# Performance work log

Hardware: AMD Instinct MI355X
Metric: run time of the kernel (lower is better)

The kernel has to match this reference:

```python
import jax, jax.numpy as jnp
import numpy as np

N, E, D, G = 50000, 600000, 128, 64
EPS = 1e-5


def prelu(x, a):
    return jnp.where(x >= 0, x, a * x)


def degree_norms(edge_src, edge_dst):
    ones = jnp.ones((E,), jnp.float32)
    deg_out = jax.ops.segment_sum(ones, edge_src, num_segments=N)
    deg_in = jax.ops.segment_sum(ones, edge_dst, num_segments=N)
    norm_src = jnp.where(deg_out > 0, jax.lax.rsqrt(jnp.maximum(deg_out, 1.0)), 0.0)
    norm_dst = jnp.where(deg_in > 0, jax.lax.rsqrt(jnp.maximum(deg_in, 1.0)), 0.0)
    return norm_src, norm_dst


def graph_conv(x, W, b, alpha, edge_src, edge_dst, norm_src, norm_dst):
    # DGL GraphConv norm='both': D_out^{-1/2} on src, aggregate, D_in^{-1/2} on dst, then linear
    xs = x * norm_src[:, None]
    agg = jax.ops.segment_sum(xs[edge_src], edge_dst, num_segments=N)
    agg = agg * norm_dst[:, None]
    h = agg @ W + b
    return prelu(h, alpha)


def batch_norm(h, gamma, beta):
    mean = jnp.mean(h, axis=0)
    var = jnp.mean(jnp.square(h - mean), axis=0)
    return (h - mean) * jax.lax.rsqrt(var + EPS) * gamma + beta


def setup_inputs() -> dict:
    key = jax.random.key(0)
    ks = jax.random.split(key, 8)
    inp = {
        "heat": jax.random.normal(ks[0], (N, D), jnp.float32),
        "edge_src": jax.random.randint(ks[1], (E,), 0, N, jnp.int32),
        "edge_dst": jax.random.randint(ks[2], (E,), 0, N, jnp.int32),
        "graph_ids": jnp.sort(jax.random.randint(ks[3], (N,), 0, G, jnp.int32)),
    }
    for i in range(2):
        kw = jax.random.fold_in(ks[4], i)
        inp[f"W{i}"] = jax.random.normal(kw, (D, D), jnp.float32) * (1.0 / np.sqrt(D))
        inp[f"b{i}"] = jnp.zeros((D,), jnp.float32)
        inp[f"ac{i}"] = jnp.float32(0.25)  # conv PReLU alpha
        inp[f"g{i}"] = jnp.ones((D,), jnp.float32)
        inp[f"be{i}"] = jnp.zeros((D,), jnp.float32)
        inp[f"aa{i}"] = jnp.float32(0.25)  # outer PReLU alpha
    return inp


def reference(heat, edge_src, edge_dst, graph_ids,
              W0, b0, ac0, g0, be0, aa0,
              W1, b1, ac1, g1, be1, aa1):
    norm_src, norm_dst = degree_norms(edge_src, edge_dst)
    x = heat  # dropout in eval mode -> identity
    h = graph_conv(x, W0, b0, ac0, edge_src, edge_dst, norm_src, norm_dst)
    h = prelu(batch_norm(h, g0, be0), aa0)
    gh = jax.ops.segment_sum(h, graph_ids, num_segments=G)
    h = graph_conv(h, W1, b1, ac1, edge_src, edge_dst, norm_src, norm_dst)
    h = prelu(batch_norm(h, g1, be1), aa1)
    gh = gh + jax.ops.segment_sum(h, graph_ids, num_segments=G)
    return h, gh
```

## Files before the change

### kernel.cpp

```cpp
#include <hip/hip_runtime.h>
#include <hip/hip_fp8.h>

#define NN 50000
#define NE 600000
#define DD 128
#define GG 64
#define EPS 1e-5f
#define CAP 64
#define HB 60
#define ECHUNK 10000
#define NPARTS 8
#define HALFP 6250
#define HWORDSP 3125
#define ZROW 50000
#define NBUILD ((NE + 255) / 256)
#define HB0 NBUILD
#define WB0 (NBUILD + NPARTS * HB)
#define NWTB 128
#define NPB (NN * 16 / 256)

typedef unsigned short u16;
typedef unsigned int u32;
typedef unsigned char u8;
typedef u16 u16x8 __attribute__((ext_vector_type(8)));
typedef u8 u8x16 __attribute__((ext_vector_type(16)));
typedef u8 u8x8 __attribute__((ext_vector_type(8)));
typedef short bf16x8 __attribute__((ext_vector_type(8)));
typedef float f32x4 __attribute__((ext_vector_type(4)));

__device__ __forceinline__ float bf2f(u16 v) {
    return __uint_as_float(((u32)v) << 16);
}
__device__ __forceinline__ u16 f2bf(float f) {
    u32 u = __float_as_uint(f);
    u += 0x7fff + ((u >> 16) & 1);
    return (u16)(u >> 16);
}
__device__ __forceinline__ float f8tof(u8 b) {
    __hip_fp8_e4m3 v;
    v.__x = b;
    return (float)v;
}
__device__ __forceinline__ u8 ftof8(float f) {
    return __hip_fp8_e4m3(f).__x;
}

__global__ __launch_bounds__(256) void k_prep(
        const int* __restrict__ src, const int* __restrict__ dst,
        u32* __restrict__ partials, int* __restrict__ cnt_in, u16* __restrict__ csr,
        const float* __restrict__ W0, const float* __restrict__ W1,
        u16* __restrict__ wtb, u8* __restrict__ xsb) {
    __shared__ u32 hc[HWORDSP];
    int blk = blockIdx.x;
    int t = threadIdx.x;
    if (blk < NBUILD) {
        int e = blk * 256 + t;
        if (e < NE) {
            int d = dst[e];
            int pos = atomicAdd(&cnt_in[d], 1);
            if (pos < CAP) csr[(size_t)d * CAP + pos] = (u16)src[e];
        }
        return;
    }
    if (blk >= WB0) {
        int gt = (blk - WB0) * 256 + t;
        int lay = gt >> 14;
        int rem = gt & 16383;
        int c = rem >> 7, k = rem & 127;
        const float* W = lay ? W1 : W0;
        wtb[lay * DD * DD + c * DD + k] = f2bf(W[k * DD + c]);
        if (gt < 16) {
            u8x8 z = {0, 0, 0, 0, 0, 0, 0, 0};
            *(u8x8*)(xsb + (size_t)ZROW * DD + gt * 8) = z;
        }
        return;
    }
    int hb = blk - HB0;
    int b = hb % HB, p = hb / HB;
    for (int i = t; i < HWORDSP; i += 256) hc[i] = 0;
    __syncthreads();
    int lo = p * HALFP;
    int e0 = b * ECHUNK;
    for (int e = e0 + t; e < e0 + ECHUNK; e += 256) {
        int s = src[e] - lo;
        if ((u32)s < (u32)HALFP) atomicAdd(&hc[s >> 1], 1u << ((s & 1) << 4));
    }
    __syncthreads();
    u32* outp = partials + (size_t)(p * HB + b) * HWORDSP;
    for (int i = t; i < HWORDSP; i += 256) outp[i] = hc[i];
}

__global__ __launch_bounds__(256) void k_scale_rows(
        const u32* __restrict__ partials, const float* __restrict__ x,
        float* __restrict__ norm_src, u8* __restrict__ xsb,
        float* __restrict__ gh, float* __restrict__ stats) {
    __shared__ float snorm[16];
    int blk = blockIdx.x;
    int t = threadIdx.x;
    if (blk < 32) {
        gh[blk * 256 + t] = 0.f;
    } else if (blk == 32) {
        stats[t] = 0.f;
        stats[256 + t] = 0.f;
    }
    int rb = blk * 16;
    int s = t >> 5, c = t & 31;
    int rA = rb + 2 * s;
    int p = rA / HALFP;
    int j = (rA - p * HALFP) >> 1;
    u32 sum = 0;
    for (int b = c; b < HB; b += 32)
        sum += partials[(size_t)(p * HB + b) * HWORDSP + j];
    sum += __shfl_xor((int)sum, 1);
    sum += __shfl_xor((int)sum, 2);
    sum += __shfl_xor((int)sum, 4);
    sum += __shfl_xor((int)sum, 8);
    sum += __shfl_xor((int)sum, 16);
    if (c == 0) {
        u32 c0 = sum & 0xffffu, c1 = sum >> 16;
        float n0 = c0 ? rsqrtf((float)c0) : 0.f;
        float n1 = c1 ? rsqrtf((float)c1) : 0.f;
        snorm[2 * s] = n0;
        snorm[2 * s + 1] = n1;
        norm_src[rA] = n0;
        norm_src[rA + 1] = n1;
    }
    __syncthreads();
    int idx = blk * 256 + t;
    int row = idx >> 4;
    int c8 = (idx & 15) << 3;
    float ns = snorm[t >> 4];
    const float4* xp = (const float4*)(x + (size_t)row * DD + c8);
    float4 a = xp[0], b2 = xp[1];
    u8x8 o;
    o[0] = ftof8(a.x * ns); o[1] = ftof8(a.y * ns); o[2] = ftof8(a.z * ns); o[3] = ftof8(a.w * ns);
    o[4] = ftof8(b2.x * ns); o[5] = ftof8(b2.y * ns); o[6] = ftof8(b2.z * ns); o[7] = ftof8(b2.w * ns);
    *(u8x8*)(xsb + (size_t)row * DD + c8) = o;
}

#define LOADF8(v, ii)                                                    \
    u8x16 v##0 = *(const u8x16*)(xcol + (size_t)(ii)[0] * DD);           \
    u8x16 v##1 = *(const u8x16*)(xcol + (size_t)(ii)[1] * DD);           \
    u8x16 v##2 = *(const u8x16*)(xcol + (size_t)(ii)[2] * DD);           \
    u8x16 v##3 = *(const u8x16*)(xcol + (size_t)(ii)[3] * DD);           \
    u8x16 v##4 = *(const u8x16*)(xcol + (size_t)(ii)[4] * DD);           \
    u8x16 v##5 = *(const u8x16*)(xcol + (size_t)(ii)[5] * DD);           \
    u8x16 v##6 = *(const u8x16*)(xcol + (size_t)(ii)[6] * DD);           \
    u8x16 v##7 = *(const u8x16*)(xcol + (size_t)(ii)[7] * DD);

#define ACCF8(acc, v)                                                    \
    _Pragma("unroll")                                                    \
    for (int j = 0; j < 16; ++j) {                                       \
        float a01 = f8tof(v##0[j]) + f8tof(v##1[j]);                     \
        float a23 = f8tof(v##2[j]) + f8tof(v##3[j]);                     \
        float a45 = f8tof(v##4[j]) + f8tof(v##5[j]);                     \
        float a67 = f8tof(v##6[j]) + f8tof(v##7[j]);                     \
        acc[j] += (a01 + a23) + (a45 + a67);                             \
    }

__global__ __launch_bounds__(256) void k_gg(
        const u8* __restrict__ xsb, const int* __restrict__ cnt_in,
        const u16* __restrict__ csr,
        const u16* __restrict__ wtb, const float* __restrict__ bias,
        const float* __restrict__ ac, u16* __restrict__ hpreb,
        float* __restrict__ sums, float* __restrict__ sumsq) {
    __shared__ u16 sAg[4][16][DD + 8];
    __shared__ float sStat[2][4][DD];
    int t = threadIdx.x;
    int w = t >> 6;
    int l = t & 63;
    int rb = blockIdx.x * 64 + w * 16;
    bool wvalid = (rb < NN);
    int cl8 = l & 7;
    int rw = l >> 3;
    const u8* xcol = xsb + cl8 * 16;

    if (wvalid) {
#pragma unroll
        for (int gp = 0; gp < 2; ++gp) {
            int r = rb + gp * 8 + rw;
            int craw = cnt_in[r];
            int cnt = min(craw, CAP);
            const u16* ce = csr + (size_t)r * CAP;
            float acc[16];
#pragma unroll
            for (int j = 0; j < 16; ++j) acc[j] = 0.f;
            int e = 0;
            for (; e + 8 <= cnt; e += 8) {
                u16x8 ii = *(const u16x8*)(ce + e);
                LOADF8(va, ii)
                ACCF8(acc, va)
            }
            if (e < cnt) {
                u16x8 ii = *(const u16x8*)(ce + e);
                int jj[8];
#pragma unroll
                for (int j = 0; j < 8; ++j) jj[j] = (e + j < cnt) ? (int)ii[j] : ZROW;
                LOADF8(vm, jj)
                ACCF8(acc, vm)
            }
            float nd = craw > 0 ? rsqrtf((float)craw) : 0.f;
            u16x8 o0, o1;
#pragma unroll
            for (int j = 0; j < 8; ++j) {
                o0[j] = f2bf(acc[j] * nd);
                o1[j] = f2bf(acc[8 + j] * nd);
            }
            *(u16x8*)&sAg[w][gp * 8 + rw][cl8 * 16] = o0;
            *(u16x8*)&sAg[w][gp * 8 + rw][cl8 * 16 + 8] = o1;
        }
    }
    __syncthreads();

    int lr = l & 15;
    int kg = l >> 4;
    float alpha = ac[0];

    bf16x8 afrag[4];
    if (wvalid) {
        const u16* abase = &sAg[w][lr][kg * 8];
        afrag[0] = *(const bf16x8*)(abase);
        afrag[1] = *(const bf16x8*)(abase + 32);
        afrag[2] = *(const bf16x8*)(abase + 64);
        afrag[3] = *(const bf16x8*)(abase + 96);
    }

#pragma unroll
    for (int ct = 0; ct < 8; ++ct) {
        int c = ct * 16;
        float sS = 0.f, sQ = 0.f;
        if (wvalid) {
            const u16* bbase = wtb + (size_t)(c + lr) * DD + kg * 8;
            bf16x8 b0 = *(const bf16x8*)(bbase);
            bf16x8 b1 = *(const bf16x8*)(bbase + 32);
            bf16x8 b2 = *(const bf16x8*)(bbase + 64);
            bf16x8 b3 = *(const bf16x8*)(bbase + 96);
            float bv = bias[c + lr];
            f32x4 acc = {bv, bv, bv, bv};
            acc = __builtin_amdgcn_mfma_f32_16x16x32_bf16(afrag[0], b0, acc, 0, 0, 0);
            acc = __builtin_amdgcn_mfma_f32_16x16x32_bf16(afrag[1], b1, acc, 0, 0, 0);
            acc = __builtin_amdgcn_mfma_f32_16x16x32_bf16(afrag[2], b2, acc, 0, 0, 0);
            acc = __builtin_amdgcn_mfma_f32_16x16x32_bf16(afrag[3], b3, acc, 0, 0, 0);
#pragma unroll
            for (int j = 0; j < 4; ++j) {
                float h = acc[j];
                h = h >= 0.f ? h : alpha * h;
                u16 hb = f2bf(h);
                float hq = bf2f(hb);
                int grow = rb + kg * 4 + j;
                hpreb[(size_t)grow * DD + c + lr] = hb;
                sS += hq;
                sQ += hq * hq;
            }
        }
        sS += __shfl_xor(sS, 16); sS += __shfl_xor(sS, 32);
        sQ += __shfl_xor(sQ, 16); sQ += __shfl_xor(sQ, 32);
        if (kg == 0) {
            sStat[0][w][c + lr] = sS;
            sStat[1][w][c + lr] = sQ;
        }
    }
    __syncthreads();
    if (t < DD) {
        float s = sStat[0][0][t] + sStat[0][1][t] + sStat[0][2][t] + sStat[0][3][t];
        atomicAdd(&sums[t], s);
    } else if (t < 2 * DD) {
        int c = t - DD;
        float q = sStat[1][0][c] + sStat[1][1][c] + sStat[1][2][c] + sStat[1][3][c];
        atomicAdd(&sumsq[c], q);
    }
}

__global__ __launch_bounds__(256) void k_post(
        const u16* __restrict__ hpreb,
        const float* __restrict__ sums, const float* __restrict__ sumsq,
        const float* __restrict__ gamma, const float* __restrict__ beta,
        const float* __restrict__ aa, const float* __restrict__ nsrc,
        float* __restrict__ h_out, u8* __restrict__ xs_next, int lastLayer,
        const int* __restrict__ gids, float* __restrict__ gh) {
    __shared__ float sc[DD], sh[DD];
    __shared__ float red[2][DD];
    int t = threadIdx.x;
    if (t < DD) {
        float mean = sums[t] * (1.0f / NN);
        float var = sumsq[t] * (1.0f / NN) - mean * mean;
        float inv = rsqrtf(var + EPS);
        float s = inv * gamma[t];
        sc[t] = s;
        sh[t] = beta[t] - mean * s;
    }
    __syncthreads();
    float a = aa[0];
    int blk = blockIdx.x;

    if (blk < NPB) {
        int idx = blk * 256 + t;
        int row = idx >> 4;
        int c8 = (idx & 15) << 3;
        u16x8 hv = *(const u16x8*)(hpreb + (size_t)idx * 8);
        float v[8];
#pragma unroll
        for (int j = 0; j < 8; ++j) v[j] = bf2f(hv[j]) * sc[c8 + j] + sh[c8 + j];
#pragma unroll
        for (int j = 0; j < 8; ++j) v[j] = v[j] >= 0.f ? v[j] : a * v[j];
        if (lastLayer) {
            float4* op = (float4*)(h_out + (size_t)idx * 8);
            op[0] = make_float4(v[0], v[1], v[2], v[3]);
            op[1] = make_float4(v[4], v[5], v[6], v[7]);
        } else {
            float ns = nsrc[row];
            u8x8 o;
#pragma unroll
            for (int j = 0; j < 8; ++j) o[j] = ftof8(v[j] * ns);
            *(u8x8*)(xs_next + (size_t)row * DD + c8) = o;
        }
        return;
    }

    int sb = blk - NPB;
    int g = sb & (GG - 1);
    int slice = sb >> 6;
    int lo, hi;
    {
        int l = 0, r = NN;
        while (l < r) { int m = (l + r) >> 1; if (gids[m] < g) l = m + 1; else r = m; }
        lo = l;
        r = NN;
        while (l < r) { int m = (l + r) >> 1; if (gids[m] < g + 1) l = m + 1; else r = m; }
        hi = l;
    }
    int cnt = hi - lo;
    int chunk = (cnt + 7) >> 3;
    int s0 = lo + slice * chunk;
    int s1 = min(s0 + chunk, hi);
    int c = t & 127;
    int half = t >> 7;
    float s = 0.f;
    for (int row = s0 + half; row < s1; row += 2) {
        float v = bf2f(hpreb[(size_t)row * DD + c]) * sc[c] + sh[c];
        v = v >= 0.f ? v : a * v;
        s += v;
    }
    red[half][c] = s;
    __syncthreads();
    if (t < DD)
        atomicAdd(&gh[g * DD + t], red[0][t] + red[1][t]);
}

extern "C" void kernel_launch(void* const* d_in, const int* in_sizes, int n_in,
                              void* d_out, int out_size, void* d_ws, size_t ws_size,
                              hipStream_t stream) {
    const float* heat = (const float*)d_in[0];
    const int* esrc = (const int*)d_in[1];
    const int* edst = (const int*)d_in[2];
    const int* gids = (const int*)d_in[3];
    const float* Wp[2]  = {(const float*)d_in[4],  (const float*)d_in[10]};
    const float* bp[2]  = {(const float*)d_in[5],  (const float*)d_in[11]};
    const float* acp[2] = {(const float*)d_in[6],  (const float*)d_in[12]};
    const float* gp[2]  = {(const float*)d_in[7],  (const float*)d_in[13]};
    const float* bep[2] = {(const float*)d_in[8],  (const float*)d_in[14]};
    const float* aap[2] = {(const float*)d_in[9],  (const float*)d_in[15]};

    float* out = (float*)d_out;
    float* h_out = out;
    float* gh = out + (size_t)NN * DD;

    char* wsp = (char*)d_ws;
    int* cnt_in_i   = (int*)wsp;              wsp += NN * sizeof(int);
    float* stats    = (float*)wsp;            wsp += 4 * DD * sizeof(float);
    float* norm_src = (float*)wsp;            wsp += NN * sizeof(float);
    u16* wtb        = (u16*)wsp;              wsp += 2 * DD * DD * sizeof(u16);
    u8* xsb         = (u8*)wsp;               wsp += (size_t)(NN + 1) * DD;
    u16* hpreb      = (u16*)wsp;              wsp += (size_t)NN * DD * sizeof(u16);
    u16* csr        = (u16*)wsp;              wsp += (size_t)NN * CAP * sizeof(u16);
    u32* partials   = (u32*)wsp;              wsp += (size_t)NPARTS * HB * HWORDSP * sizeof(u32);

    hipMemsetAsync(cnt_in_i, 0, NN * sizeof(int), stream);

    k_prep<<<WB0 + NWTB, 256, 0, stream>>>(esrc, edst, partials, cnt_in_i, csr,
                                           Wp[0], Wp[1], wtb, xsb);
    k_scale_rows<<<NPB, 256, 0, stream>>>(partials, heat, norm_src, xsb, gh, stats);

    for (int layer = 0; layer < 2; ++layer) {
        float* sums_l  = stats + layer * 2 * DD;
        float* sumsq_l = sums_l + DD;
        k_gg<<<(NN + 63) / 64, 256, 0, stream>>>(xsb, cnt_in_i, csr,
                                                 wtb + layer * DD * DD, bp[layer], acp[layer],
                                                 hpreb, sums_l, sumsq_l);
        k_post<<<NPB + GG * 8, 256, 0, stream>>>(hpreb, sums_l, sumsq_l,
                                                 gp[layer], bep[layer], aap[layer],
                                                 norm_src, h_out, xsb, layer == 1 ? 1 : 0,
                                                 gids, gh);
    }
}
```

Baseline: 202.7 us.

## Build dst CSR via LDS histograms and prefix offsets instead of global atomics

```diff
diff --git a/kernel.cpp b/kernel.cpp
--- a/kernel.cpp
+++ b/kernel.cpp
@@ -13,9 +13,8 @@
 #define HALFP 6250
 #define HWORDSP 3125
 #define ZROW 50000
-#define NBUILD ((NE + 255) / 256)
-#define HB0 NBUILD
-#define WB0 (NBUILD + NPARTS * HB)
+#define NHIST (NPARTS * HB)
+#define WB0 (2 * NHIST)
 #define NWTB 128
 #define NPB (NN * 16 / 256)
 
@@ -47,21 +46,12 @@
 
 __global__ __launch_bounds__(256) void k_prep(
         const int* __restrict__ src, const int* __restrict__ dst,
-        u32* __restrict__ partials, int* __restrict__ cnt_in, u16* __restrict__ csr,
+        u32* __restrict__ psrc, u32* __restrict__ pdst,
         const float* __restrict__ W0, const float* __restrict__ W1,
         u16* __restrict__ wtb, u8* __restrict__ xsb) {
     __shared__ u32 hc[HWORDSP];
     int blk = blockIdx.x;
     int t = threadIdx.x;
-    if (blk < NBUILD) {
-        int e = blk * 256 + t;
-        if (e < NE) {
-            int d = dst[e];
-            int pos = atomicAdd(&cnt_in[d], 1);
-            if (pos < CAP) csr[(size_t)d * CAP + pos] = (u16)src[e];
-        }
-        return;
-    }
     if (blk >= WB0) {
         int gt = (blk - WB0) * 256 + t;
         int lay = gt >> 14;
@@ -75,26 +65,30 @@
         }
         return;
     }
-    int hb = blk - HB0;
+    int kind = blk >= NHIST;
+    int hb = kind ? blk - NHIST : blk;
     int b = hb % HB, p = hb / HB;
+    const int* __restrict__ arr = kind ? dst : src;
     for (int i = t; i < HWORDSP; i += 256) hc[i] = 0;
     __syncthreads();
     int lo = p * HALFP;
     int e0 = b * ECHUNK;
     for (int e = e0 + t; e < e0 + ECHUNK; e += 256) {
-        int s = src[e] - lo;
-        if ((u32)s < (u32)HALFP) atomicAdd(&hc[s >> 1], 1u << ((s & 1) << 4));
-    }
-    __syncthreads();
-    u32* outp = partials + (size_t)(p * HB + b) * HWORDSP;
+        int v = arr[e] - lo;
+        if ((u32)v < (u32)HALFP) atomicAdd(&hc[v >> 1], 1u << ((v & 1) << 4));
+    }
+    __syncthreads();
+    u32* outp = (kind ? pdst : psrc) + (size_t)(p * HB + b) * HWORDSP;
     for (int i = t; i < HWORDSP; i += 256) outp[i] = hc[i];
 }
 
 __global__ __launch_bounds__(256) void k_scale_rows(
-        const u32* __restrict__ partials, const float* __restrict__ x,
+        const u32* __restrict__ psrc, u32* __restrict__ pdst,
+        const float* __restrict__ x, int* __restrict__ cnt_in,
         float* __restrict__ norm_src, u8* __restrict__ xsb,
         float* __restrict__ gh, float* __restrict__ stats) {
     __shared__ float snorm[16];
+    __shared__ u32 stage[8][HB];
     int blk = blockIdx.x;
     int t = threadIdx.x;
     if (blk < 32) {
@@ -104,13 +98,40 @@
         stats[256 + t] = 0.f;
     }
     int rb = blk * 16;
+    for (int i = t; i < 8 * HB; i += 256) {
+        int s = i & 7, b = i >> 3;
+        int rA = rb + 2 * s;
+        int p = rA / HALFP;
+        int j = (rA - p * HALFP) >> 1;
+        stage[s][b] = pdst[(size_t)(p * HB + b) * HWORDSP + j];
+    }
+    __syncthreads();
+    if (t < 8) {
+        u32 run = 0;
+        for (int b = 0; b < HB; ++b) {
+            u32 v = stage[t][b];
+            stage[t][b] = run;
+            run += v;
+        }
+        int rA = rb + 2 * t;
+        cnt_in[rA] = (int)(run & 0xffffu);
+        cnt_in[rA + 1] = (int)(run >> 16);
+    }
+    __syncthreads();
+    for (int i = t; i < 8 * HB; i += 256) {
+        int s = i & 7, b = i >> 3;
+        int rA = rb + 2 * s;
+        int p = rA / HALFP;
+        int j = (rA - p * HALFP) >> 1;
+        pdst[(size_t)(p * HB + b) * HWORDSP + j] = stage[s][b];
+    }
     int s = t >> 5, c = t & 31;
     int rA = rb + 2 * s;
     int p = rA / HALFP;
     int j = (rA - p * HALFP) >> 1;
     u32 sum = 0;
     for (int b = c; b < HB; b += 32)
-        sum += partials[(size_t)(p * HB + b) * HWORDSP + j];
+        sum += psrc[(size_t)(p * HB + b) * HWORDSP + j];
     sum += __shfl_xor((int)sum, 1);
     sum += __shfl_xor((int)sum, 2);
     sum += __shfl_xor((int)sum, 4);
@@ -136,6 +157,29 @@
     o[0] = ftof8(a.x * ns); o[1] = ftof8(a.y * ns); o[2] = ftof8(a.z * ns); o[3] = ftof8(a.w * ns);
     o[4] = ftof8(b2.x * ns); o[5] = ftof8(b2.y * ns); o[6] = ftof8(b2.z * ns); o[7] = ftof8(b2.w * ns);
     *(u8x8*)(xsb + (size_t)row * DD + c8) = o;
+}
+
+__global__ __launch_bounds__(256) void k_place(
+        const int* __restrict__ src, const int* __restrict__ dst,
+        const u32* __restrict__ pdst, u16* __restrict__ csr) {
+    __shared__ u32 ctr[HWORDSP];
+    int b = blockIdx.x % HB, p = blockIdx.x / HB;
+    int t = threadIdx.x;
+    const u32* basep = pdst + (size_t)(p * HB + b) * HWORDSP;
+    for (int i = t; i < HWORDSP; i += 256) ctr[i] = basep[i];
+    __syncthreads();
+    int lo = p * HALFP;
+    int e0 = b * ECHUNK;
+    for (int e = e0 + t; e < e0 + ECHUNK; e += 256) {
+        int d = dst[e];
+        int v = d - lo;
+        if ((u32)v < (u32)HALFP) {
+            int sh = (v & 1) << 4;
+            u32 old = atomicAdd(&ctr[v >> 1], 1u << sh);
+            u32 pos = (old >> sh) & 0xffffu;
+            if (pos < CAP) csr[(size_t)d * CAP + pos] = (u16)src[e];
+        }
+    }
 }
 
 #define LOADF8(v, ii)                                                    \
@@ -373,13 +417,14 @@
     u8* xsb         = (u8*)wsp;               wsp += (size_t)(NN + 1) * DD;
     u16* hpreb      = (u16*)wsp;              wsp += (size_t)NN * DD * sizeof(u16);
     u16* csr        = (u16*)wsp;              wsp += (size_t)NN * CAP * sizeof(u16);
-    u32* partials   = (u32*)wsp;              wsp += (size_t)NPARTS * HB * HWORDSP * sizeof(u32);
-
-    hipMemsetAsync(cnt_in_i, 0, NN * sizeof(int), stream);
-
-    k_prep<<<WB0 + NWTB, 256, 0, stream>>>(esrc, edst, partials, cnt_in_i, csr,
+    u32* psrc       = (u32*)wsp;              wsp += (size_t)NPARTS * HB * HWORDSP * sizeof(u32);
+    u32* pdst       = (u32*)wsp;              wsp += (size_t)NPARTS * HB * HWORDSP * sizeof(u32);
+
+    k_prep<<<WB0 + NWTB, 256, 0, stream>>>(esrc, edst, psrc, pdst,
                                            Wp[0], Wp[1], wtb, xsb);
-    k_scale_rows<<<NPB, 256, 0, stream>>>(partials, heat, norm_src, xsb, gh, stats);
+    k_scale_rows<<<NPB, 256, 0, stream>>>(psrc, pdst, heat, cnt_in_i,
+                                          norm_src, xsb, gh, stats);
+    k_place<<<NHIST, 256, 0, stream>>>(esrc, edst, pdst, csr);
 
     for (int layer = 0; layer < 2; ++layer) {
         float* sums_l  = stats + layer * 2 * DD;
```

New measurement: 210.2 us, median of 4. 1.04x slower.
